# Performance work log

Measured on AMD Instinct MI355X. Metric: run time of the kernel, lower is better.

The kernel has to match this reference:

```python
import jax, jax.numpy as jnp
import numpy as np
from jax import lax

DIM = 192
HEADS = 8
B, H, W = 8, 128, 128


def dwconv3x3(x, w):
    # x: [B,C,H,W], w: [C,1,3,3] depthwise (groups=C)
    return lax.conv_general_dilated(
        x, w, window_strides=(1, 1), padding='SAME',
        feature_group_count=x.shape[1],
        dimension_numbers=('NCHW', 'OIHW', 'NCHW'))


def conv1x1(x, w, b=None):
    # w: [Cout, Cin]
    y = jnp.einsum('oc,bchw->bohw', w, x)
    if b is not None:
        y = y + b[None, :, None, None]
    return y


def setup_inputs() -> dict:
    key = jax.random.key(0)
    ks = jax.random.split(key, 9)
    s = 0.02
    return {
        'x': jax.random.normal(ks[0], (B, DIM, H, W), jnp.float32),
        'w_qkv': jax.random.normal(ks[1], (3 * DIM, DIM), jnp.float32) * s,
        'b_qkv': jnp.zeros((3 * DIM,), jnp.float32),
        'w_dw': jax.random.normal(ks[2], (3 * DIM, 1, 3, 3), jnp.float32) * s,
        'b_dw': jnp.zeros((3 * DIM,), jnp.float32),
        'w_proj': jax.random.normal(ks[3], (DIM, DIM), jnp.float32) * s,
        'b_proj': jnp.zeros((DIM,), jnp.float32),
        'w_pos1': jax.random.normal(ks[4], (DIM, 1, 3, 3), jnp.float32) * s,
        'w_pos2': jax.random.normal(ks[5], (DIM, 1, 3, 3), jnp.float32) * s,
        'temperature': jnp.ones((HEADS, 1, 1), jnp.float32),
    }


def reference(x, w_qkv, b_qkv, w_dw, b_dw, w_proj, b_proj, w_pos1, w_pos2, temperature):
    b, c, h, w = x.shape
    heads = HEADS
    ch = c // heads

    qkv = conv1x1(x, w_qkv, b_qkv)
    qkv = dwconv3x3(qkv, w_dw) + b_dw[None, :, None, None]
    q_inp, k_inp, v_inp = jnp.split(qkv, 3, axis=1)

    def to_heads(t):  # [B,C,H,W] -> [B,heads,ch,HW]
        return t.reshape(b, heads, ch, h * w)

    q = to_heads(q_inp)
    k = to_heads(k_inp)
    v = to_heads(v_inp)

    # L2 normalize over hw (torch F.normalize, eps=1e-12)
    q = q / jnp.maximum(jnp.linalg.norm(q, axis=-1, keepdims=True), 1e-12)
    k = k / jnp.maximum(jnp.linalg.norm(k, axis=-1, keepdims=True), 1e-12)

    attn = jnp.einsum('bhce,bhde->bhcd', q, k) * temperature  # [B,heads,ch,ch]
    attn = jax.nn.softmax(attn, axis=-1)
    out = jnp.einsum('bhcd,bhde->bhce', attn, v)  # [B,heads,ch,HW]
    out = out.reshape(b, c, h, w)

    out = conv1x1(out, w_proj, b_proj)

    pos = dwconv3x3(v_inp, w_pos1)
    pos = jax.nn.gelu(pos, approximate=False)
    pos = dwconv3x3(pos, w_pos2)

    return out + pos
```

## Files before the change

kernel.cpp:

```cpp
#include <hip/hip_runtime.h>
#include <stdint.h>
#include <stddef.h>

#define NB 8
#define CC 192
#define C3 576
#define HGT 128
#define WID 128
#define HW 16384
#define NH 8
#define QKROW 49152

typedef short bf16x8 __attribute__((ext_vector_type(8)));
typedef float f32x4 __attribute__((ext_vector_type(4)));

__device__ __forceinline__ unsigned short f2bf(float f) {
  unsigned int u = __float_as_uint(f);
  u += 0x7fffu + ((u >> 16) & 1u);
  return (unsigned short)(u >> 16);
}
__device__ __forceinline__ float bf2f(unsigned short h) {
  return __uint_as_float(((unsigned int)h) << 16);
}
__device__ __forceinline__ float bflo(unsigned int v) {
  return __uint_as_float(v << 16);
}
__device__ __forceinline__ float bfhi(unsigned int v) {
  return __uint_as_float(v & 0xffff0000u);
}
__device__ __forceinline__ unsigned int pk2(float a, float b) {
  return (unsigned int)f2bf(a) | ((unsigned int)f2bf(b) << 16);
}
__device__ __forceinline__ void gl_lds16(const void* g, void* l) {
  __builtin_amdgcn_global_load_lds(
      (const __attribute__((address_space(1))) unsigned int*)(uintptr_t)g,
      (__attribute__((address_space(3))) unsigned int*)(uint32_t)(uintptr_t)l,
      16, 0, 0);
}
__device__ __forceinline__ int xcd_swz(int g, int n) {
  return (g & 7) * (n >> 3) + (g >> 3);
}

__global__ void kwprep(const float* __restrict__ wq, unsigned char* __restrict__ wb) {
  int f = blockIdx.x * 256 + threadIdx.x;
  if (f >= C3 * 24) return;
  int oc = f / 24, s = f % 24;
  unsigned int wv[4];
#pragma unroll
  for (int j = 0; j < 4; ++j)
    wv[j] = pk2(wq[oc * 192 + s * 8 + 2 * j], wq[oc * 192 + s * 8 + 2 * j + 1]);
  uint4 st; st.x = wv[0]; st.y = wv[1]; st.z = wv[2]; st.w = wv[3];
  *(uint4*)(wb + (size_t)oc * 384 + ((s ^ (oc & 7)) * 16)) = st;
}

__global__ __launch_bounds__(256) void kqkv(const float* __restrict__ x,
                                            const unsigned char* __restrict__ wb,
                                            const float* __restrict__ bqkv,
                                            unsigned short* __restrict__ vout,
                                            unsigned char* __restrict__ qkout) {
  __shared__ __align__(16) unsigned char lds[81920];
  const int ABF = 49152;
  const int TRO = 73728;
  int wg = xcd_swz(blockIdx.x, gridDim.x);
  int t = wg & 255, b = wg >> 8;
  int p0 = t * 64;
  int tid = threadIdx.x;

  const unsigned char* gx = (const unsigned char*)(x + (size_t)b * CC * HW + p0);
#pragma unroll
  for (int i = 0; i < 12; ++i) {
    int f = i * 256 + tid;
    int ch = f >> 4, seg = f & 15;
    gl_lds16(gx + ((size_t)ch * HW + seg * 4) * 4, lds + f * 16);
  }
  asm volatile("s_waitcnt vmcnt(0)" ::: "memory");
  __syncthreads();
  {
    const float* lx = (const float*)lds;
    int p = tid & 63, sg = tid >> 6;
#pragma unroll
    for (int s6 = 0; s6 < 6; ++s6) {
      int s = sg * 6 + s6;
      unsigned int wv[4];
#pragma unroll
      for (int j = 0; j < 4; ++j)
        wv[j] = pk2(lx[(s * 8 + 2 * j) * 64 + p], lx[(s * 8 + 2 * j + 1) * 64 + p]);
      uint4 st; st.x = wv[0]; st.y = wv[1]; st.z = wv[2]; st.w = wv[3];
      *(uint4*)(lds + ABF + (s * 64 + p) * 16) = st;
    }
  }
  __syncthreads();

#pragma unroll
  for (int i = 0; i < 6; ++i)
    gl_lds16(wb + i * 4096 + tid * 16, lds + i * 4096 + tid * 16);

  int lane = tid & 63, w = tid >> 6;
  int l15 = lane & 15, gq = lane >> 4;
  int pw = w * 16;
  int y = t >> 1, xh = (t & 1) * 8;
  int unitw = w * 2 + (gq >> 1);
  int sub8 = (gq & 1) * 8;
  int s4 = w * 4 + gq;
  int ru = tid >> 5, rc0 = tid & 31;
  int vc = tid >> 2, vxq = tid & 3;

  for (int ot = 0; ot < 9; ++ot) {
    if (ot == 0) { asm volatile("s_waitcnt vmcnt(0)" ::: "memory"); }
    else         { asm volatile("s_waitcnt vmcnt(2)" ::: "memory"); }
    __builtin_amdgcn_s_barrier();
    __builtin_amdgcn_sched_barrier(0);
    int nb = ot & 1;
    float bias[4];
#pragma unroll
    for (int nf = 0; nf < 4; ++nf) bias[nf] = bqkv[ot * 64 + nf * 16 + l15];
    if (ot < 8) {
      const unsigned char* gB = wb + (size_t)(ot + 1) * 24576;
#pragma unroll
      for (int i = 0; i < 6; ++i)
        gl_lds16(gB + i * 4096 + tid * 16, lds + (nb ^ 1) * 24576 + i * 4096 + tid * 16);
    }
    f32x4 acc[4];
#pragma unroll
    for (int nf = 0; nf < 4; ++nf) acc[nf] = (f32x4){0.f, 0.f, 0.f, 0.f};
#pragma unroll
    for (int kk = 0; kk < 6; ++kk) {
      bf16x8 a = *(const bf16x8*)(lds + ABF + (((kk * 4 + gq) * 64) + pw + l15) * 16);
      int cb = kk * 64 + gq * 16;
#pragma unroll
      for (int nf = 0; nf < 4; ++nf) {
        int r = nf * 16 + l15;
        bf16x8 bfr = *(const bf16x8*)(lds + nb * 24576 + r * 384 + (cb ^ ((r & 7) << 4)));
        acc[nf] = __builtin_amdgcn_mfma_f32_16x16x32_bf16(a, bfr, acc[nf], 0, 0, 0);
      }
    }
    bool isq = (ot < 6);
    if (isq) {
#pragma unroll
      for (int nf = 0; nf < 4; ++nf) {
        int c = nf * 16 + l15;
        uint2 st;
        st.x = pk2(acc[nf][0] + bias[nf], acc[nf][1] + bias[nf]);
        st.y = pk2(acc[nf][2] + bias[nf], acc[nf][3] + bias[nf]);
        *(uint2*)(lds + TRO + c * 128 + ((unitw ^ (c & 7)) * 16) + sub8) = st;
      }
    } else {
#pragma unroll
      for (int nf = 0; nf < 4; ++nf) {
        int c = nf * 16 + l15;
        uint2 st;
        st.x = pk2(acc[nf][0] + bias[nf], acc[nf][1] + bias[nf]);
        st.y = pk2(acc[nf][2] + bias[nf], acc[nf][3] + bias[nf]);
        *(uint2*)(lds + TRO + c * 128 + ((s4 ^ (c & 15)) * 8)) = st;
      }
    }
    asm volatile("s_waitcnt lgkmcnt(0)" ::: "memory");
    __builtin_amdgcn_s_barrier();
    __builtin_amdgcn_sched_barrier(0);
    if (isq) {
      int part = ot / 3, cm0 = (ot % 3) * 64;
      int c1 = rc0 + 32;
      uint4 v0 = *(const uint4*)(lds + TRO + rc0 * 128 + ((ru ^ (rc0 & 7)) * 16));
      uint4 v1 = *(const uint4*)(lds + TRO + c1 * 128 + ((ru ^ (c1 & 7)) * 16));
      unsigned char* grow = qkout + ((size_t)((part * 8 + b) * 128 + y)) * QKROW +
                            (xh + ru) * 3072 + cm0 * 16;
      *(uint4*)(grow + rc0 * 16) = v0;
      *(uint4*)(grow + c1 * 16) = v1;
    } else {
      uint2 q0 = *(const uint2*)(lds + TRO + vc * 128 + (((4 * vxq + 0) ^ (vc & 15)) * 8));
      uint2 q1 = *(const uint2*)(lds + TRO + vc * 128 + (((4 * vxq + 1) ^ (vc & 15)) * 8));
      uint2 q2 = *(const uint2*)(lds + TRO + vc * 128 + (((4 * vxq + 2) ^ (vc & 15)) * 8));
      uint2 q3 = *(const uint2*)(lds + TRO + vc * 128 + (((4 * vxq + 3) ^ (vc & 15)) * 8));
      unsigned short* vp = vout + ((size_t)(b * CC + (ot - 6) * 64 + vc)) * HW + p0 + vxq * 16;
      uint4 s0; s0.x = q0.x; s0.y = q0.y; s0.z = q1.x; s0.w = q1.y;
      uint4 s1; s1.x = q2.x; s1.y = q2.y; s1.z = q3.x; s1.w = q3.y;
      *(uint4*)vp = s0;
      *(uint4*)(vp + 8) = s1;
    }
  }
}

__global__ __launch_bounds__(256) void kqk(const unsigned char* __restrict__ qk,
                                           const float* __restrict__ wdw,
                                           const float* __restrict__ bdw,
                                           float* __restrict__ G,
                                           float* __restrict__ nq,
                                           float* __restrict__ nk) {
  __shared__ __align__(16) unsigned char lds[81920];
  const int FB = 49152;
  int wg = xcd_swz(blockIdx.x, gridDim.x);
  int band = wg & 63, h = (wg >> 6) & 7, b = wg >> 9;
  int y0 = band * 2;
  int tid = threadIdx.x;
#pragma unroll
  for (int i = 0; i < 12; ++i) {
    int f = i * 256 + tid;
    int p = f / 1536, rem = f % 1536;
    int r = rem / 384, unit = rem % 384;
    int uc = unit / 24, ch = unit % 24;
    int y = y0 - 1 + r;
    if (y >= 0 && y < HGT)
      gl_lds16(qk + ((size_t)((p * 8 + b) * 128 + y)) * QKROW + uc * 3072 + (h * 24 + ch) * 16,
               lds + f * 16);
    else
      *(uint4*)(lds + f * 16) = (uint4){0, 0, 0, 0};
  }
  asm volatile("s_waitcnt vmcnt(0)" ::: "memory");
  __syncthreads();

  int lane = tid & 63, w = tid >> 6;
  if (tid < 192) {
    int p = tid / 96; int r3m = tid % 96;
    int ch = r3m >> 2; int row = (r3m >> 1) & 1; int half = r3m & 1;
    int gc = p * 192 + h * 24 + ch;
    float wv[9];
#pragma unroll
    for (int j = 0; j < 9; ++j) wv[j] = wdw[gc * 9 + j];
    float bias = bdw[gc];
    const unsigned char* sbase = lds + p * 24576 + ch * 16;
    unsigned char* fb = lds + FB + p * 16384 + ch * 16;
    int h8 = half * 8;
    unsigned int W[3][16];
#define LOADU(dy_, m_, u_) { \
    uint4 tt = ((u_) >= 0 && (u_) < 16) \
        ? *(const uint4*)(sbase + (row + (dy_)) * 6144 + (u_) * 384) \
        : (uint4){0, 0, 0, 0}; \
    W[dy_][(m_) * 4 + 0] = tt.x; W[dy_][(m_) * 4 + 1] = tt.y; \
    W[dy_][(m_) * 4 + 2] = tt.z; W[dy_][(m_) * 4 + 3] = tt.w; }
#pragma unroll
    for (int dy = 0; dy < 3; ++dy) {
#pragma unroll
      for (int m = 0; m < 4; ++m) { LOADU(dy, m, h8 - 1 + m); }
    }
    float nsum = 0.f;
#pragma unroll
    for (int c4 = 0; c4 < 4; ++c4) {
      if (c4 > 0) {
#pragma unroll
        for (int dy = 0; dy < 3; ++dy) {
#pragma unroll
          for (int e = 0; e < 8; ++e) W[dy][e] = W[dy][8 + e];
          LOADU(dy, 2, h8 - 1 + c4 * 2 + 2);
          LOADU(dy, 3, h8 - 1 + c4 * 2 + 3);
        }
      }
      float acc[16];
#pragma unroll
      for (int j = 0; j < 16; ++j) acc[j] = bias;
#pragma unroll
      for (int dy = 0; dy < 3; ++dy) {
        float f[18];
#pragma unroll
        for (int t2 = 0; t2 < 18; ++t2) {
          int rel = 7 + t2;
          unsigned int v = W[dy][rel >> 1];
          f[t2] = (rel & 1) ? bfhi(v) : bflo(v);
        }
#pragma unroll
        for (int j = 0; j < 16; ++j)
          acc[j] += f[j] * wv[dy * 3] + f[j + 1] * wv[dy * 3 + 1] + f[j + 2] * wv[dy * 3 + 2];
      }
#pragma unroll
      for (int j = 0; j < 16; ++j) nsum += acc[j] * acc[j];
      unsigned int pk[8];
#pragma unroll
      for (int e = 0; e < 8; ++e) pk[e] = pk2(acc[2 * e], acc[2 * e + 1]);
      int kt = row * 4 + half * 2 + (c4 >> 1);
      int gb = (c4 & 1) * 2;
      uint4 s0; s0.x = pk[0]; s0.y = pk[1]; s0.z = pk[2]; s0.w = pk[3];
      uint4 s1; s1.x = pk[4]; s1.y = pk[5]; s1.z = pk[6]; s1.w = pk[7];
      *(uint4*)(fb + kt * 2048 + gb * 512) = s0;
      *(uint4*)(fb + kt * 2048 + (gb + 1) * 512) = s1;
    }
#undef LOADU
    nsum += __shfl_xor(nsum, 1);
    nsum += __shfl_xor(nsum, 2);
    if ((tid & 3) == 0) {
      float* dst = (p == 0) ? nq : nk;
      atomicAdd(dst + (b * NH + h) * 24 + ch, nsum);
    }
  } else {
    int t2 = tid - 192;
#pragma unroll
    for (int i = 0; i < 8; ++i) {
      int f = i * 64 + t2;
      int ch8 = f & 7, gq4 = (f >> 3) & 3, kt8 = (f >> 5) & 7, pp = f >> 8;
      *(uint4*)(lds + FB + pp * 16384 + kt8 * 2048 + gq4 * 512 + (24 + ch8) * 16) =
          (uint4){0, 0, 0, 0};
    }
  }
  __syncthreads();

  int l15 = lane & 15, gq = lane >> 4;
  f32x4 acc2[2][2];
#pragma unroll
  for (int ct = 0; ct < 2; ++ct)
#pragma unroll
    for (int dt = 0; dt < 2; ++dt) acc2[ct][dt] = (f32x4){0.f, 0.f, 0.f, 0.f};
#pragma unroll
  for (int t2 = 0; t2 < 2; ++t2) {
    int kt = w * 2 + t2;
    bf16x8 aq[2], bk[2];
#pragma unroll
    for (int ct = 0; ct < 2; ++ct) {
      aq[ct] = *(const bf16x8*)(lds + FB + kt * 2048 + gq * 512 + (ct * 16 + l15) * 16);
      bk[ct] = *(const bf16x8*)(lds + FB + 16384 + kt * 2048 + gq * 512 + (ct * 16 + l15) * 16);
    }
#pragma unroll
    for (int ct = 0; ct < 2; ++ct)
#pragma unroll
      for (int dt = 0; dt < 2; ++dt)
        acc2[ct][dt] = __builtin_amdgcn_mfma_f32_16x16x32_bf16(aq[ct], bk[dt], acc2[ct][dt], 0, 0, 0);
  }
  float* gp = (float*)lds;
#pragma unroll
  for (int ct = 0; ct < 2; ++ct)
#pragma unroll
    for (int dt = 0; dt < 2; ++dt)
      *(f32x4*)(gp + (((w * 4 + ct * 2 + dt) * 64) + lane) * 4) = acc2[ct][dt];
  __syncthreads();
  float* Gb = G + (size_t)(b * NH + h) * 576;
#pragma unroll
  for (int ii = 0; ii < 3; ++ii) {
    int f = ii * 256 + tid;
    if (f < 576) {
      int c = f / 24, d = f % 24;
      int t4 = ((c >> 4) << 1) + (d >> 4);
      int lane16 = (d & 15) + (((c & 15) >> 2) << 4);
      int reg = c & 3;
      float s = 0.f;
#pragma unroll
      for (int w4 = 0; w4 < 4; ++w4)
        s += gp[((w4 * 4 + t4) * 64 + lane16) * 4 + reg];
      atomicAdd(Gb + f, s);
    }
  }
}

__global__ __launch_bounds__(256) void kdwv(const unsigned short* __restrict__ src,
                                            const float* __restrict__ wdw,
                                            const float* __restrict__ bdw,
                                            unsigned char* __restrict__ vT) {
  __shared__ __align__(16) unsigned int smem[8 * 721];
  int wg = xcd_swz(blockIdx.x, gridDim.x);
  int cg = wg % 24, rt = (wg / 24) & 15, b = wg / 384;
  int y0 = rt * 8, chg0 = cg * 8;
  int tid = threadIdx.x;
  for (int i = tid; i < 5768; i += 256) smem[i] = 0;
  __syncthreads();
#pragma unroll
  for (int i = 0; i < 5; ++i) {
    int f = i * 256 + tid;
    int ch = f / 160, rem = f % 160;
    int r = rem >> 4, seg = rem & 15;
    int y = y0 - 1 + r;
    if (y >= 0 && y < HGT) {
      uint4 v = *(const uint4*)(src + ((size_t)(b * CC + chg0 + ch)) * HW + y * WID + seg * 8);
      unsigned int* dp = smem + ch * 721 + r * 72 + 4 + seg * 4;
      dp[0] = v.x; dp[1] = v.y; dp[2] = v.z; dp[3] = v.w;
    }
  }
  __syncthreads();
  int ch = tid >> 5, u = tid & 31;
  int row = u >> 2, xs = (u & 3) * 32;
  int gch = 384 + chg0 + ch;
  float wv[9];
#pragma unroll
  for (int j = 0; j < 9; ++j) wv[j] = wdw[gch * 9 + j];
  float bias = bdw[gch];
  float outv[32];
  const unsigned int* tb = smem + ch * 721;
#pragma unroll
  for (int g = 0; g < 4; ++g) {
    int x0 = xs + g * 8;
    float v[3][12];
#pragma unroll
    for (int dy = 0; dy < 3; ++dy) {
      const unsigned int* rp = tb + (row + dy) * 72 + ((x0 + 6) >> 1);
#pragma unroll
      for (int m = 0; m < 6; ++m) {
        unsigned int w2 = rp[m];
        v[dy][2 * m] = bf2f((unsigned short)(w2 & 0xffff));
        v[dy][2 * m + 1] = bf2f((unsigned short)(w2 >> 16));
      }
    }
#pragma unroll
    for (int j = 0; j < 8; ++j) {
      float a = bias;
#pragma unroll
      for (int dy = 0; dy < 3; ++dy)
#pragma unroll
        for (int dx = 0; dx < 3; ++dx)
          a += v[dy][j + dx + 1] * wv[dy * 3 + dx];
      outv[g * 8 + j] = a;
    }
  }
  __syncthreads();
  unsigned short* vt = (unsigned short*)smem;
#pragma unroll
  for (int g = 0; g < 4; ++g)
#pragma unroll
    for (int j = 0; j < 8; j += 2) {
      int x = xs + g * 8 + j;
      ((unsigned int*)smem)[ch * 512 + row * 64 + (x >> 1)] =
          pk2(outv[g * 8 + j], outv[g * 8 + j + 1]);
    }
  __syncthreads();
#pragma unroll
  for (int i = 0; i < 4; ++i) {
    int f = i * 256 + tid;
    int r = f >> 7, col = f & 127;
    unsigned int wvp[4];
#pragma unroll
    for (int e = 0; e < 4; ++e) {
      unsigned short a = vt[(2 * e) * 1024 + r * 128 + col];
      unsigned short bb = vt[(2 * e + 1) * 1024 + r * 128 + col];
      wvp[e] = (unsigned int)a | ((unsigned int)bb << 16);
    }
    uint4 st; st.x = wvp[0]; st.y = wvp[1]; st.z = wvp[2]; st.w = wvp[3];
    *(uint4*)(vT + (((size_t)(b * 24 + cg)) * HW + (size_t)(y0 + r) * WID + col) * 16) = st;
  }
}

__global__ __launch_bounds__(256) void kattn(const float* __restrict__ G,
                                             const float* __restrict__ nq,
                                             const float* __restrict__ nk,
                                             const float* __restrict__ temp,
                                             const float* __restrict__ wproj,
                                             unsigned char* __restrict__ W2) {
  __shared__ float attn[24][24];
  __shared__ float iq[24], ik[24];
  int bh = blockIdx.x;
  int h = bh & 7, b = bh >> 3;
  int tid = threadIdx.x;
  const float* Gb = G + (size_t)bh * 576;
  if (tid < 24) { float n = sqrtf(nq[bh * 24 + tid]); iq[tid] = 1.f / fmaxf(n, 1e-12f); }
  else if (tid < 48) { float n = sqrtf(nk[bh * 24 + tid - 24]); ik[tid - 24] = 1.f / fmaxf(n, 1e-12f); }
  __syncthreads();
  if (tid < 24) {
    float tmp = temp[h];
    float row[24];
    float mx = -1e30f;
#pragma unroll
    for (int d = 0; d < 24; ++d) {
      row[d] = Gb[tid * 24 + d] * iq[tid] * ik[d] * tmp;
      mx = fmaxf(mx, row[d]);
    }
    float sum = 0.f;
#pragma unroll
    for (int d = 0; d < 24; ++d) { float e = expf(row[d] - mx); row[d] = e; sum += e; }
    float inv = 1.f / sum;
#pragma unroll
    for (int d = 0; d < 24; ++d) attn[tid][d] = row[d] * inv;
  }
  __syncthreads();
  for (int i = 0; i < 18; ++i) {
    int f = tid + i * 256;
    if (f >= 4608) break;
    int oc = f / 24, d = f % 24;
    float s = 0.f;
#pragma unroll
    for (int c = 0; c < 24; ++c) s += wproj[oc * 192 + h * 24 + c] * attn[c][d];
    int gg = h * 24 + d;
    *(unsigned short*)(W2 + ((size_t)b * CC + oc) * 384 + ((gg * 2) ^ ((oc & 7) << 4))) = f2bf(s);
  }
}

__global__ __launch_bounds__(256) void kpos(const unsigned char* __restrict__ vT,
                                            const float* __restrict__ w1,
                                            const float* __restrict__ w2,
                                            unsigned short* __restrict__ pos) {
  __shared__ unsigned int vbuf[8 * 865];
  __shared__ unsigned int d1[8 * 721];
  int wg = xcd_swz(blockIdx.x, gridDim.x);
  int cg = wg % 24, rt = (wg / 24) & 15, b = wg / 384;
  int y0 = rt * 8, g0 = cg * 8;
  int tid = threadIdx.x;
  for (int i = tid; i < 6920; i += 256) vbuf[i] = 0;
  __syncthreads();
#pragma unroll
  for (int i = 0; i < 3; ++i) {
    int f = i * 256 + tid;
    int r = f >> 6, colp = f & 63;
    int y = y0 - 2 + r;
    if (y >= 0 && y < HGT) {
      const unsigned char* base = vT + (((size_t)(b * 24 + cg)) * HW + (size_t)y * WID + colp * 2) * 16;
      uint4 va = *(const uint4*)(base);
      uint4 vb2 = *(const uint4*)(base + 16);
      unsigned int la[4] = {va.x, va.y, va.z, va.w};
      unsigned int lb[4] = {vb2.x, vb2.y, vb2.z, vb2.w};
#pragma unroll
      for (int e = 0; e < 8; ++e) {
        unsigned int a16 = (la[e >> 1] >> ((e & 1) * 16)) & 0xffff;
        unsigned int b16 = (lb[e >> 1] >> ((e & 1) * 16)) & 0xffff;
        vbuf[e * 865 + r * 72 + colp + 4] = a16 | (b16 << 16);
      }
    }
  }
  __syncthreads();
  int ch = tid >> 5, u = tid & 31;
  {
    const float* wp = w1 + (g0 + ch) * 9;
    float wl[9];
#pragma unroll
    for (int j = 0; j < 9; ++j) wl[j] = wp[j];
    int x0 = u * 4;
    for (int rr = 0; rr < 10; ++rr) {
      int y = y0 - 1 + rr;
      unsigned int o0 = 0, o1 = 0;
      if (y >= 0 && y < HGT) {
        float v[3][8];
#pragma unroll
        for (int dy = 0; dy < 3; ++dy) {
          const unsigned int* rp = vbuf + ch * 865 + (rr + dy) * 72 + ((x0 + 6) >> 1);
#pragma unroll
          for (int m = 0; m < 4; ++m) {
            unsigned int w2r = rp[m];
            v[dy][2 * m] = bf2f((unsigned short)(w2r & 0xffff));
            v[dy][2 * m + 1] = bf2f((unsigned short)(w2r >> 16));
          }
        }
        float g4[4];
#pragma unroll
        for (int j = 0; j < 4; ++j) {
          float a = 0.f;
#pragma unroll
          for (int dy = 0; dy < 3; ++dy)
#pragma unroll
            for (int dx = 0; dx < 3; ++dx)
              a += v[dy][j + dx + 1] * wl[dy * 3 + dx];
          g4[j] = 0.5f * a * (1.f + erff(a * 0.70710678118f));
        }
        o0 = pk2(g4[0], g4[1]);
        o1 = pk2(g4[2], g4[3]);
      }
      unsigned int* dp = d1 + ch * 721 + rr * 72 + ((x0 + 8) >> 1);
      dp[0] = o0; dp[1] = o1;
    }
  }
  if (tid < 160) {
    int ech = tid / 20, rem = tid % 20;
    int rr = rem >> 1, side = rem & 1;
    int x = side ? 128 : -1;
    int y = y0 - 1 + rr;
    unsigned short val = 0;
    if (y >= 0 && y < HGT) {
      const float* wp = w1 + (g0 + ech) * 9;
      float a = 0.f;
      const unsigned short* vb16 = (const unsigned short*)(vbuf + ech * 865);
#pragma unroll
      for (int dy = 0; dy < 3; ++dy)
#pragma unroll
        for (int dx = 0; dx < 3; ++dx)
          a += bf2f(vb16[(rr + dy) * 144 + (x + dx + 7)]) * wp[dy * 3 + dx];
      val = f2bf(0.5f * a * (1.f + erff(a * 0.70710678118f)));
    }
    ((unsigned short*)(d1 + ech * 721))[rr * 144 + (x + 8)] = val;
  }
  __syncthreads();
  {
    const float* wp = w2 + (g0 + ch) * 9;
    float wl[9];
#pragma unroll
    for (int j = 0; j < 9; ++j) wl[j] = wp[j];
    int row = u >> 2, xs = (u & 3) * 32;
    size_t rb = ((size_t)(b * CC + g0 + ch)) * HW + (size_t)(y0 + row) * WID;
#pragma unroll
    for (int g = 0; g < 4; ++g) {
      int x0 = xs + g * 8;
      float v[3][12];
#pragma unroll
      for (int dy = 0; dy < 3; ++dy) {
        const unsigned int* rp = d1 + ch * 721 + (row + dy) * 72 + ((x0 + 6) >> 1);
#pragma unroll
        for (int m = 0; m < 6; ++m) {
          unsigned int w2r = rp[m];
          v[dy][2 * m] = bf2f((unsigned short)(w2r & 0xffff));
          v[dy][2 * m + 1] = bf2f((unsigned short)(w2r >> 16));
        }
      }
      uint4 st;
      float o[8];
#pragma unroll
      for (int j = 0; j < 8; ++j) {
        float a = 0.f;
#pragma unroll
        for (int dy = 0; dy < 3; ++dy)
#pragma unroll
          for (int dx = 0; dx < 3; ++dx)
            a += v[dy][j + dx + 1] * wl[dy * 3 + dx];
        o[j] = a;
      }
      st.x = pk2(o[0], o[1]); st.y = pk2(o[2], o[3]);
      st.z = pk2(o[4], o[5]); st.w = pk2(o[6], o[7]);
      *(uint4*)(pos + rb + x0) = st;
    }
  }
}

__global__ __launch_bounds__(256) void kproj(const unsigned char* __restrict__ vT,
                                             const unsigned char* __restrict__ W2,
                                             const float* __restrict__ bproj,
                                             const unsigned short* __restrict__ pos,
                                             float* __restrict__ out) {
  __shared__ __align__(16) unsigned char lds[73728];
  int wg = xcd_swz(blockIdx.x, gridDim.x);
  int ot = wg % 3; int rest = wg / 3; int grp = rest & 63; int b = rest >> 6;
  int tid = threadIdx.x;
  const unsigned char* gB = W2 + ((size_t)(b * 192 + ot * 64)) * 384;
#pragma unroll
  for (int i = 0; i < 6; ++i)
    gl_lds16(gB + i * 4096 + tid * 16, lds + 49152 + i * 4096 + tid * 16);
  const unsigned char* gA = vT + (size_t)b * 24 * HW * 16;
  int t0 = grp * 4;
  {
    int p0 = t0 * 64;
#pragma unroll
    for (int i = 0; i < 6; ++i) {
      int f = i * 256 + tid;
      gl_lds16(gA + (((size_t)(f >> 6)) * HW + p0 + (f & 63)) * 16, lds + f * 16);
    }
  }
  int lane = tid & 63, w = tid >> 6;
  int l15 = lane & 15, gq = lane >> 4;
  int pw = w * 16;
  float bias[4];
  size_t obase[4];
#pragma unroll
  for (int nf = 0; nf < 4; ++nf) {
    int oc = ot * 64 + nf * 16 + l15;
    bias[nf] = bproj[oc];
    obase[nf] = ((size_t)(b * 192 + oc)) * HW;
  }
  for (int it = 0; it < 4; ++it) {
    int tile = t0 + it;
    asm volatile("s_waitcnt vmcnt(0)" ::: "memory");
    __syncthreads();
    int nb = it & 1;
    if (it < 3) {
      int p1 = (tile + 1) * 64;
#pragma unroll
      for (int i = 0; i < 6; ++i) {
        int f = i * 256 + tid;
        gl_lds16(gA + (((size_t)(f >> 6)) * HW + p1 + (f & 63)) * 16,
                 lds + ((nb ^ 1) * 24576) + f * 16);
      }
    }
    f32x4 acc[4];
#pragma unroll
    for (int nf = 0; nf < 4; ++nf) acc[nf] = (f32x4){0.f, 0.f, 0.f, 0.f};
#pragma unroll
    for (int kk = 0; kk < 6; ++kk) {
      bf16x8 a = *(const bf16x8*)(lds + nb * 24576 + ((((kk * 4 + gq) << 6) + pw + l15) * 16));
      int cb = kk * 64 + gq * 16;
#pragma unroll
      for (int nf = 0; nf < 4; ++nf) {
        int r = nf * 16 + l15;
        bf16x8 bfr = *(const bf16x8*)(lds + 49152 + r * 384 + (cb ^ ((r & 7) << 4)));
        acc[nf] = __builtin_amdgcn_mfma_f32_16x16x32_bf16(a, bfr, acc[nf], 0, 0, 0);
      }
    }
    int p = tile * 64 + pw + gq * 4;
#pragma unroll
    for (int nf = 0; nf < 4; ++nf) {
      uint2 pv = *(const uint2*)(pos + obase[nf] + p);
      float4 o;
      o.x = acc[nf][0] + bias[nf] + bf2f((unsigned short)(pv.x & 0xffff));
      o.y = acc[nf][1] + bias[nf] + bf2f((unsigned short)(pv.x >> 16));
      o.z = acc[nf][2] + bias[nf] + bf2f((unsigned short)(pv.y & 0xffff));
      o.w = acc[nf][3] + bias[nf] + bf2f((unsigned short)(pv.y >> 16));
      *(float4*)(out + obase[nf] + p) = o;
    }
  }
}

#define OFF_W   ((size_t)0)
#define OFF_G   ((size_t)221184)
#define OFF_NQ  ((size_t)368640)
#define OFF_NK  ((size_t)374784)
#define OFF_W2  ((size_t)380928)
#define OFF_QK  ((size_t)970752)
#define OFF_V   ((size_t)101634048)
#define OFF_XT  ((size_t)151965696)

extern "C" void kernel_launch(void* const* d_in, const int* in_sizes, int n_in,
                              void* d_out, int out_size, void* d_ws, size_t ws_size,
                              hipStream_t stream) {
  const float* x     = (const float*)d_in[0];
  const float* wqkv  = (const float*)d_in[1];
  const float* bqkv  = (const float*)d_in[2];
  const float* wdw   = (const float*)d_in[3];
  const float* bdw   = (const float*)d_in[4];
  const float* wproj = (const float*)d_in[5];
  const float* bproj = (const float*)d_in[6];
  const float* wpos1 = (const float*)d_in[7];
  const float* wpos2 = (const float*)d_in[8];
  const float* temp  = (const float*)d_in[9];
  unsigned char* ws = (unsigned char*)d_ws;

  hipMemsetAsync(ws + OFF_G, 0, 147456 + 6144 + 6144, stream);
  kwprep<<<54, 256, 0, stream>>>(wqkv, ws + OFF_W);
  kqkv<<<2048, 256, 0, stream>>>(x, ws + OFF_W, bqkv,
                                 (unsigned short*)(ws + OFF_V), ws + OFF_QK);
  kqk<<<4096, 256, 0, stream>>>(ws + OFF_QK, wdw, bdw, (float*)(ws + OFF_G),
                                (float*)(ws + OFF_NQ), (float*)(ws + OFF_NK));
  kdwv<<<3072, 256, 0, stream>>>((const unsigned short*)(ws + OFF_V), wdw, bdw,
                                 ws + OFF_XT);
  kattn<<<64, 256, 0, stream>>>((const float*)(ws + OFF_G), (const float*)(ws + OFF_NQ),
                                (const float*)(ws + OFF_NK), temp, wproj, ws + OFF_W2);
  kpos<<<3072, 256, 0, stream>>>(ws + OFF_XT, wpos1, wpos2,
                                 (unsigned short*)(ws + OFF_QK));
  kproj<<<1536, 256, 0, stream>>>(ws + OFF_XT, ws + OFF_W2, bproj,
                                  (const unsigned short*)(ws + OFF_QK), (float*)d_out);
}
```

Before: 289.3 us.

## Shrink kqk LDS footprint by staging q and k sequentially with compact layout

The kqk kernel now stages the q and k input bands one at a time into a shared staging region and packs the convolved bf16 tiles densely (24 channels instead of 32), using a single zero slot for the padded MFMA lanes. This cuts shared memory from about 80KB to about 48KB per block, so more blocks can be resident per CU. The depthwise work is also redistributed across threads as 8 per channel instead of 4. The cost is an extra sync and load phase per block and less overlap between the q and k loads.

```diff
diff --git a/kernel.cpp b/kernel.cpp
--- a/kernel.cpp
+++ b/kernel.cpp
@@ -186,110 +186,105 @@
                                            float* __restrict__ G,
                                            float* __restrict__ nq,
                                            float* __restrict__ nk) {
-  __shared__ __align__(16) unsigned char lds[81920];
-  const int FB = 49152;
+  __shared__ __align__(16) unsigned char lds[49168];
+  const int FB = 0;
+  const int ZP = 24576;
+  const int STG = 24592;
   int wg = xcd_swz(blockIdx.x, gridDim.x);
   int band = wg & 63, h = (wg >> 6) & 7, b = wg >> 9;
   int y0 = band * 2;
   int tid = threadIdx.x;
-#pragma unroll
-  for (int i = 0; i < 12; ++i) {
-    int f = i * 256 + tid;
-    int p = f / 1536, rem = f % 1536;
-    int r = rem / 384, unit = rem % 384;
-    int uc = unit / 24, ch = unit % 24;
-    int y = y0 - 1 + r;
-    if (y >= 0 && y < HGT)
-      gl_lds16(qk + ((size_t)((p * 8 + b) * 128 + y)) * QKROW + uc * 3072 + (h * 24 + ch) * 16,
-               lds + f * 16);
-    else
-      *(uint4*)(lds + f * 16) = (uint4){0, 0, 0, 0};
-  }
-  asm volatile("s_waitcnt vmcnt(0)" ::: "memory");
-  __syncthreads();
+  if (tid == 0) *(uint4*)(lds + ZP) = (uint4){0, 0, 0, 0};
 
   int lane = tid & 63, w = tid >> 6;
-  if (tid < 192) {
-    int p = tid / 96; int r3m = tid % 96;
-    int ch = r3m >> 2; int row = (r3m >> 1) & 1; int half = r3m & 1;
-    int gc = p * 192 + h * 24 + ch;
-    float wv[9];
-#pragma unroll
-    for (int j = 0; j < 9; ++j) wv[j] = wdw[gc * 9 + j];
-    float bias = bdw[gc];
-    const unsigned char* sbase = lds + p * 24576 + ch * 16;
-    unsigned char* fb = lds + FB + p * 16384 + ch * 16;
-    int h8 = half * 8;
-    unsigned int W[3][16];
-#define LOADU(dy_, m_, u_) { \
+  int ch = tid >> 3, row = (tid >> 2) & 1, qt = tid & 3;
+  int u0 = qt * 4;
+
+#pragma unroll
+  for (int p = 0; p < 2; ++p) {
+#pragma unroll
+    for (int i = 0; i < 6; ++i) {
+      int f = i * 256 + tid;
+      int r = f / 384, unit = f % 384;
+      int uc = unit / 24, cs = unit % 24;
+      int yy = y0 - 1 + r;
+      if (yy >= 0 && yy < HGT)
+        gl_lds16(qk + ((size_t)((p * 8 + b) * 128 + yy)) * QKROW + uc * 3072 + (h * 24 + cs) * 16,
+                 lds + STG + f * 16);
+      else
+        *(uint4*)(lds + STG + f * 16) = (uint4){0, 0, 0, 0};
+    }
+    asm volatile("s_waitcnt vmcnt(0)" ::: "memory");
+    __syncthreads();
+    if (tid < 192) {
+      int gc = p * 192 + h * 24 + ch;
+      float wv[9];
+#pragma unroll
+      for (int j = 0; j < 9; ++j) wv[j] = wdw[gc * 9 + j];
+      float bias = bdw[gc];
+      const unsigned char* sbase = lds + STG + ch * 16;
+      unsigned char* fb = lds + FB + p * 12288 + (row * 4 + qt) * 1536 + ch * 16;
+      unsigned int W[3][16];
+#define LOADU3(dy_, m_, u_) { \
     uint4 tt = ((u_) >= 0 && (u_) < 16) \
         ? *(const uint4*)(sbase + (row + (dy_)) * 6144 + (u_) * 384) \
         : (uint4){0, 0, 0, 0}; \
     W[dy_][(m_) * 4 + 0] = tt.x; W[dy_][(m_) * 4 + 1] = tt.y; \
     W[dy_][(m_) * 4 + 2] = tt.z; W[dy_][(m_) * 4 + 3] = tt.w; }
 #pragma unroll
-    for (int dy = 0; dy < 3; ++dy) {
-#pragma unroll
-      for (int m = 0; m < 4; ++m) { LOADU(dy, m, h8 - 1 + m); }
-    }
-    float nsum = 0.f;
-#pragma unroll
-    for (int c4 = 0; c4 < 4; ++c4) {
-      if (c4 > 0) {
+      for (int dy = 0; dy < 3; ++dy) {
+#pragma unroll
+        for (int m = 0; m < 4; ++m) { LOADU3(dy, m, u0 - 1 + m); }
+      }
+      float nsum = 0.f;
+#pragma unroll
+      for (int c4 = 0; c4 < 2; ++c4) {
+        if (c4 > 0) {
+#pragma unroll
+          for (int dy = 0; dy < 3; ++dy) {
+#pragma unroll
+            for (int e = 0; e < 8; ++e) W[dy][e] = W[dy][8 + e];
+            LOADU3(dy, 2, u0 + 3);
+            LOADU3(dy, 3, u0 + 4);
+          }
+        }
+        float acc[16];
+#pragma unroll
+        for (int j = 0; j < 16; ++j) acc[j] = bias;
 #pragma unroll
         for (int dy = 0; dy < 3; ++dy) {
-#pragma unroll
-          for (int e = 0; e < 8; ++e) W[dy][e] = W[dy][8 + e];
-          LOADU(dy, 2, h8 - 1 + c4 * 2 + 2);
-          LOADU(dy, 3, h8 - 1 + c4 * 2 + 3);
+          float f[18];
+#pragma unroll
+          for (int t2 = 0; t2 < 18; ++t2) {
+            int rel = 7 + t2;
+            unsigned int v = W[dy][rel >> 1];
+            f[t2] = (rel & 1) ? bfhi(v) : bflo(v);
+          }
+#pragma unroll
+          for (int j = 0; j < 16; ++j)
+            acc[j] += f[j] * wv[dy * 3] + f[j + 1] * wv[dy * 3 + 1] + f[j + 2] * wv[dy * 3 + 2];
         }
-      }
-      float acc[16];
-#pragma unroll
-      for (int j = 0; j < 16; ++j) acc[j] = bias;
-#pragma unroll
-      for (int dy = 0; dy < 3; ++dy) {
-        float f[18];
-#pragma unroll
-        for (int t2 = 0; t2 < 18; ++t2) {
-          int rel = 7 + t2;
-          unsigned int v = W[dy][rel >> 1];
-          f[t2] = (rel & 1) ? bfhi(v) : bflo(v);
-        }
-#pragma unroll
-        for (int j = 0; j < 16; ++j)
-          acc[j] += f[j] * wv[dy * 3] + f[j + 1] * wv[dy * 3 + 1] + f[j + 2] * wv[dy * 3 + 2];
-      }
-#pragma unroll
-      for (int j = 0; j < 16; ++j) nsum += acc[j] * acc[j];
-      unsigned int pk[8];
-#pragma unroll
-      for (int e = 0; e < 8; ++e) pk[e] = pk2(acc[2 * e], acc[2 * e + 1]);
-      int kt = row * 4 + half * 2 + (c4 >> 1);
-      int gb = (c4 & 1) * 2;
-      uint4 s0; s0.x = pk[0]; s0.y = pk[1]; s0.z = pk[2]; s0.w = pk[3];
-      uint4 s1; s1.x = pk[4]; s1.y = pk[5]; s1.z = pk[6]; s1.w = pk[7];
-      *(uint4*)(fb + kt * 2048 + gb * 512) = s0;
-      *(uint4*)(fb + kt * 2048 + (gb + 1) * 512) = s1;
-    }
-#undef LOADU
-    nsum += __shfl_xor(nsum, 1);
-    nsum += __shfl_xor(nsum, 2);
-    if ((tid & 3) == 0) {
-      float* dst = (p == 0) ? nq : nk;
-      atomicAdd(dst + (b * NH + h) * 24 + ch, nsum);
-    }
-  } else {
-    int t2 = tid - 192;
-#pragma unroll
-    for (int i = 0; i < 8; ++i) {
-      int f = i * 64 + t2;
-      int ch8 = f & 7, gq4 = (f >> 3) & 3, kt8 = (f >> 5) & 7, pp = f >> 8;
-      *(uint4*)(lds + FB + pp * 16384 + kt8 * 2048 + gq4 * 512 + (24 + ch8) * 16) =
-          (uint4){0, 0, 0, 0};
-    }
-  }
-  __syncthreads();
+#pragma unroll
+        for (int j = 0; j < 16; ++j) nsum += acc[j] * acc[j];
+        unsigned int pk[8];
+#pragma unroll
+        for (int e = 0; e < 8; ++e) pk[e] = pk2(acc[2 * e], acc[2 * e + 1]);
+        uint4 s0; s0.x = pk[0]; s0.y = pk[1]; s0.z = pk[2]; s0.w = pk[3];
+        uint4 s1; s1.x = pk[4]; s1.y = pk[5]; s1.z = pk[6]; s1.w = pk[7];
+        *(uint4*)(fb + (c4 * 2) * 384) = s0;
+        *(uint4*)(fb + (c4 * 2 + 1) * 384) = s1;
+      }
+#undef LOADU3
+      nsum += __shfl_xor(nsum, 1);
+      nsum += __shfl_xor(nsum, 2);
+      nsum += __shfl_xor(nsum, 4);
+      if ((tid & 7) == 0) {
+        float* dst = (p == 0) ? nq : nk;
+        atomicAdd(dst + (b * NH + h) * 24 + ch, nsum);
+      }
+    }
+    __syncthreads();
+  }
 
   int l15 = lane & 15, gq = lane >> 4;
   f32x4 acc2[2][2];
@@ -303,8 +298,13 @@
     bf16x8 aq[2], bk[2];
 #pragma unroll
     for (int ct = 0; ct < 2; ++ct) {
-      aq[ct] = *(const bf16x8*)(lds + FB + kt * 2048 + gq * 512 + (ct * 16 + l15) * 16);
-      bk[ct] = *(const bf16x8*)(lds + FB + 16384 + kt * 2048 + gq * 512 + (ct * 16 + l15) * 16);
+      int c = ct * 16 + l15;
+      const unsigned char* qa =
+          (c < 24) ? (lds + FB + kt * 1536 + gq * 384 + c * 16) : (lds + ZP);
+      const unsigned char* ka =
+          (c < 24) ? (lds + FB + 12288 + kt * 1536 + gq * 384 + c * 16) : (lds + ZP);
+      aq[ct] = *(const bf16x8*)qa;
+      bk[ct] = *(const bf16x8*)ka;
     }
 #pragma unroll
     for (int ct = 0; ct < 2; ++ct)
@@ -312,7 +312,7 @@
       for (int dt = 0; dt < 2; ++dt)
         acc2[ct][dt] = __builtin_amdgcn_mfma_f32_16x16x32_bf16(aq[ct], bk[dt], acc2[ct][dt], 0, 0, 0);
   }
-  float* gp = (float*)lds;
+  float* gp = (float*)(lds + STG);
 #pragma unroll
   for (int ct = 0; ct < 2; ++ct)
 #pragma unroll
```

Measured after the change: 287.8 us. Within noise of the previous version (-0.5%).
